# Performance work log

Measured on AMD Instinct MI355X. Metric: run time of the kernel, lower is better.

## Reference

```python
import jax, jax.numpy as jnp
import numpy as np

HIDDEN = 4096
Q_HEADS = 32
KV_HEADS = 8
HEAD_DIM = 128
MAX_LEN = 8192
PAST_LEN = 4096
SEQ_LEN = 16
BSZ = 1
REPEAT_KV = Q_HEADS // KV_HEADS
SCALE = HEAD_DIM ** (-0.5)


def _apply_rope(x):
    # x: [b, h, s, d]; positions start at 0 (faithful to source, even for cached k)
    s, d = x.shape[2], x.shape[3]
    half = d // 2
    positions = jnp.arange(s, dtype=x.dtype)
    inv_freq = jnp.arange(half, dtype=x.dtype) / half
    angles = positions[:, None] * inv_freq[None, :]          # [s, half]
    sin = jnp.sin(angles)[None, None]
    cos = jnp.cos(angles)[None, None]
    x_even, x_odd = x[..., :half], x[..., half:]
    return jnp.concatenate([x_even * cos - x_odd * sin,
                            x_even * sin + x_odd * cos], axis=-1)


def setup_inputs() -> dict:
    key = jax.random.key(0)
    ks = jax.random.split(key, 5)
    qkv_dim = (Q_HEADS + 2 * KV_HEADS) * HEAD_DIM
    x = jax.random.normal(ks[0], (BSZ, SEQ_LEN, HIDDEN), dtype=jnp.float32)
    w_qkv = jax.random.normal(ks[1], (qkv_dim, HIDDEN), dtype=jnp.float32) * 0.02
    w_out = jax.random.normal(ks[2], (HIDDEN, Q_HEADS * HEAD_DIM), dtype=jnp.float32) * 0.02
    cache_k = jax.random.normal(ks[3], (1, KV_HEADS, MAX_LEN, HEAD_DIM), dtype=jnp.float32)
    cache_v = jax.random.normal(ks[4], (1, KV_HEADS, MAX_LEN, HEAD_DIM), dtype=jnp.float32)
    return {"x": x, "w_qkv": w_qkv, "w_out": w_out, "cache_k": cache_k, "cache_v": cache_v}


def reference(x, w_qkv, w_out, cache_k, cache_v):
    bsz, seq_len, _ = x.shape
    qkv = jnp.einsum('bsh,oh->bso', x, w_qkv)
    q_size = Q_HEADS * HEAD_DIM
    kv_size = KV_HEADS * HEAD_DIM
    q = qkv[..., :q_size].reshape(bsz, seq_len, Q_HEADS, HEAD_DIM).transpose(0, 2, 1, 3)
    k = qkv[..., q_size:q_size + kv_size].reshape(bsz, seq_len, KV_HEADS, HEAD_DIM).transpose(0, 2, 1, 3)
    v = qkv[..., q_size + kv_size:].reshape(bsz, seq_len, KV_HEADS, HEAD_DIM).transpose(0, 2, 1, 3)
    q = _apply_rope(q)
    k = _apply_rope(k)
    # KV-cache append (static slice positions)
    cache_k = cache_k.at[:, :, PAST_LEN:PAST_LEN + seq_len, :].set(k)
    cache_v = cache_v.at[:, :, PAST_LEN:PAST_LEN + seq_len, :].set(v)
    key_len = PAST_LEN + seq_len
    key = cache_k[:, :, :key_len, :]
    value = cache_v[:, :, :key_len, :]
    if REPEAT_KV > 1:  # GQA broadcast
        key = jnp.repeat(key, REPEAT_KV, axis=1)
        value = jnp.repeat(value, REPEAT_KV, axis=1)
    scores = jnp.einsum('bhqd,bhkd->bhqk', q, key) * SCALE
    q_pos = jnp.arange(seq_len)
    k_pos = jnp.arange(key_len)
    mask = (k_pos[None, :] <= q_pos[:, None] + PAST_LEN).astype(scores.dtype)
    scores = scores + (1.0 - mask)[None, None] * -10000.0
    weights = jax.nn.softmax(scores, axis=-1)
    out = jnp.einsum('bhqk,bhkd->bhqd', weights, value)
    out = out.transpose(0, 2, 1, 3).reshape(bsz, seq_len, Q_HEADS * HEAD_DIM)
    return jnp.einsum('bso,ho->bsh', out, w_out)
```

## Files before the change

### kernel.cpp

```cpp
#include <hip/hip_runtime.h>
#include <hip/hip_bf16.h>

typedef __bf16 bf16;
typedef __bf16 bf16x4 __attribute__((ext_vector_type(4)));
typedef __bf16 bf16x8 __attribute__((ext_vector_type(8)));
typedef float f32x4 __attribute__((ext_vector_type(4)));

#define HID 4096
#define QKVN 6144
#define NQH 32
#define NKVH 8
#define HD 128
#define MAXLEN 8192
#define PAST 4096
#define SQ 16
#define SCALE 0.08838834764831845f
#define NEGBIG (-30000.0f)

#define KS 8
#define KPB 512
#define WSTR 520
#define ACH 64
#define NCH 65

__device__ __forceinline__ f32x4 mfma16(bf16x8 a, bf16x8 b, f32x4 c) {
  return __builtin_amdgcn_mfma_f32_16x16x32_bf16(a, b, c, 0, 0, 0);
}

__device__ __forceinline__ bf16x8 load8f(const float* p) {
  const f32x4* q = (const f32x4*)p;
  f32x4 a = q[0], b = q[1];
  bf16x8 r;
  r[0] = (bf16)a[0]; r[1] = (bf16)a[1]; r[2] = (bf16)a[2]; r[3] = (bf16)a[3];
  r[4] = (bf16)b[0]; r[5] = (bf16)b[1]; r[6] = (bf16)b[2]; r[7] = (bf16)b[3];
  return r;
}

__device__ __forceinline__ int fmidx(int k, int m) {
  return ((k >> 3) * 16 + m) * 8 + (k & 7);
}

__global__ __launch_bounds__(256) void xprep_kernel(const float* __restrict__ x,
                                                    bf16* __restrict__ xf) {
  int id = blockIdx.x * 256 + threadIdx.x;
  int m = id & 15, o = id >> 4;
  bf16x8 v = load8f(x + (size_t)m * HID + o * 8);
  *(bf16x8*)(xf + (size_t)(o * 16 + m) * 8) = v;
}

template <int NT>
__global__ __launch_bounds__(256) void gemm16_kernel(const bf16* __restrict__ afrag,
                                                     const float* __restrict__ w,
                                                     float* __restrict__ partial) {
  int tid = threadIdx.x, lane = tid & 63, wv = tid >> 6;
  int l15 = lane & 15, quad = lane >> 4;
  int nt = blockIdx.x % NT, kq = blockIdx.x / NT;

  __shared__ __align__(16) bf16 Wt[16 * WSTR];
  __shared__ __align__(16) float red[4][64][4];

  const float* wb = w + (size_t)(nt * 16) * HID + kq * KPB;
  int r2 = tid >> 7;
  int c4 = tid & 127;
  f32x4 stg[8];
#pragma unroll
  for (int it = 0; it < 8; ++it)
    stg[it] = *(const f32x4*)(wb + (size_t)(it * 2 + r2) * HID + c4 * 4);

  int obase = kq * 64 + wv * 16;
  bf16x8 af[4];
#pragma unroll
  for (int kk = 0; kk < 4; ++kk)
    af[kk] = *(const bf16x8*)(afrag + (size_t)((obase + kk * 4 + quad) * 16 + l15) * 8);

#pragma unroll
  for (int it = 0; it < 8; ++it) {
    bf16x4 t;
    t[0] = (bf16)stg[it][0]; t[1] = (bf16)stg[it][1];
    t[2] = (bf16)stg[it][2]; t[3] = (bf16)stg[it][3];
    *(bf16x4*)(Wt + (it * 2 + r2) * WSTR + c4 * 4) = t;
  }
  __syncthreads();

  f32x4 acc = {0.f, 0.f, 0.f, 0.f};
#pragma unroll
  for (int kk = 0; kk < 4; ++kk) {
    bf16x8 b = *(const bf16x8*)(Wt + l15 * WSTR + wv * 128 + kk * 32 + quad * 8);
    acc = mfma16(af[kk], b, acc);
  }

  *(f32x4*)(&red[wv][lane][0]) = acc;
  __syncthreads();
  if (wv == 0) {
#pragma unroll
    for (int r = 0; r < 4; ++r) {
      float v = red[0][lane][r] + red[1][lane][r] + red[2][lane][r] + red[3][lane][r];
      partial[((size_t)(kq * NT + nt) * 16 + (quad * 4 + r)) * 16 + l15] = v;
    }
  }
}

__device__ __forceinline__ float sum_part(const float* p, int NT, int n, int m) {
  float s = 0.f;
#pragma unroll
  for (int q = 0; q < KS; ++q)
    s += p[((size_t)(q * NT + (n >> 4)) * 16 + m) * 16 + (n & 15)];
  return s;
}

__global__ __launch_bounds__(256) void qkv_finish_kernel(const float* __restrict__ pq,
                                                         bf16* __restrict__ Qf,
                                                         bf16* __restrict__ Kf,
                                                         bf16* __restrict__ Vn) {
  int id = blockIdx.x * 256 + threadIdx.x;
  if (id < 32768) {
    int qh = id >> 10, m = (id >> 6) & 15, j = id & 63;
    float e = sum_part(pq, 384, qh * 128 + j, m);
    float o = sum_part(pq, 384, qh * 128 + 64 + j, m);
    float sn, co;
    __sincosf((float)m * (float)j * (1.0f / 64.0f), &sn, &co);
    Qf[qh * 2048 + fmidx(j, m)] = (bf16)((e * co - o * sn) * SCALE);
    Qf[qh * 2048 + fmidx(j + 64, m)] = (bf16)((e * sn + o * co) * SCALE);
  } else if (id < 40960) {
    int v = id - 32768;
    int kvh = v >> 10, m = (v >> 6) & 15, j = v & 63;
    float e = sum_part(pq, 384, 4096 + kvh * 128 + j, m);
    float o = sum_part(pq, 384, 4096 + kvh * 128 + 64 + j, m);
    float sn, co;
    __sincosf((float)m * (float)j * (1.0f / 64.0f), &sn, &co);
    Kf[kvh * 2048 + fmidx(j, m)] = (bf16)(e * co - o * sn);
    Kf[kvh * 2048 + fmidx(j + 64, m)] = (bf16)(e * sn + o * co);
  } else if (id < 57344) {
    int v = id - 40960;
    int kvh = v >> 11, m = (v >> 7) & 15, d = v & 127;
    Vn[kvh * 2048 + m * 128 + d] = (bf16)sum_part(pq, 384, 5120 + kvh * 128 + d, m);
  }
}

template <bool NEW>
__device__ void attn_body(int kvh, int c,
                          const float* __restrict__ ck, const float* __restrict__ cv,
                          const bf16* __restrict__ Qf, const bf16* __restrict__ Kf,
                          const bf16* __restrict__ Vn,
                          bf16* __restrict__ Opart, float* __restrict__ ml,
                          bf16* Kt, bf16* Vt, bf16* Pl) {
  int tid = threadIdx.x, lane = tid & 63, wv = tid >> 6;
  int l15 = lane & 15, quad = lane >> 4;
  int qh = kvh * 4 + wv;
  int cs = c * ACH;

  if (!NEW) {
    {
      int kr = tid >> 5;
      int kc4 = tid & 31;
      f32x4 kst[8];
#pragma unroll
      for (int it = 0; it < 8; ++it)
        kst[it] = *(const f32x4*)(ck + ((size_t)(kvh * MAXLEN + cs + it * 8 + kr)) * HD + kc4 * 4);
      int key = tid & 63, dg = tid >> 6;
      f32x4 vst[8];
#pragma unroll
      for (int q4 = 0; q4 < 8; ++q4)
        vst[q4] = *(const f32x4*)(cv + ((size_t)(kvh * MAXLEN + cs + key)) * HD + dg * 32 + q4 * 4);
#pragma unroll
      for (int it = 0; it < 8; ++it) {
        bf16x4 t;
        t[0] = (bf16)kst[it][0]; t[1] = (bf16)kst[it][1];
        t[2] = (bf16)kst[it][2]; t[3] = (bf16)kst[it][3];
        *(bf16x4*)(Kt + (it * 8 + kr) * 136 + kc4 * 4) = t;
      }
#pragma unroll
      for (int q4 = 0; q4 < 8; ++q4)
#pragma unroll
        for (int i = 0; i < 4; ++i)
          Vt[(dg * 32 + q4 * 4 + i) * 72 + key] = (bf16)vst[q4][i];
    }
  } else {
    int key = tid >> 4, dg8 = tid & 15;
    bf16x8 v = *(const bf16x8*)(Vn + kvh * 2048 + key * 128 + dg8 * 8);
#pragma unroll
    for (int i = 0; i < 8; ++i) {
      Vt[(dg8 * 8 + i) * 72 + key] = v[i];
      Vt[(dg8 * 8 + i) * 72 + 16 + key] = (bf16)0.f;
    }
  }
  __syncthreads();

  bf16x8 af[4];
#pragma unroll
  for (int kk = 0; kk < 4; ++kk)
    af[kk] = *(const bf16x8*)(Qf + qh * 2048 + ((kk * 4 + quad) * 16 + l15) * 8);

  constexpr int NT = NEW ? 1 : 4;
  f32x4 sc[NT];
  if (!NEW) {
#pragma unroll
    for (int nt = 0; nt < NT; ++nt) {
      f32x4 acc = {0.f, 0.f, 0.f, 0.f};
#pragma unroll
      for (int kk = 0; kk < 4; ++kk) {
        bf16x8 b = *(const bf16x8*)(Kt + (nt * 16 + l15) * 136 + kk * 32 + quad * 8);
        acc = mfma16(af[kk], b, acc);
      }
      sc[nt] = acc;
    }
  } else {
    f32x4 acc = {0.f, 0.f, 0.f, 0.f};
#pragma unroll
    for (int kk = 0; kk < 4; ++kk) {
      bf16x8 b = *(const bf16x8*)(Kf + kvh * 2048 + ((kk * 4 + quad) * 16 + l15) * 8);
      acc = mfma16(af[kk], b, acc);
    }
#pragma unroll
    for (int r = 0; r < 4; ++r)
      if (l15 > quad * 4 + r) acc[r] = NEGBIG;
    sc[0] = acc;
  }

  float mx[4], sm[4];
#pragma unroll
  for (int r = 0; r < 4; ++r) {
    float v = sc[0][r];
#pragma unroll
    for (int nt = 1; nt < NT; ++nt) v = fmaxf(v, sc[nt][r]);
    v = fmaxf(v, __shfl_xor(v, 1));
    v = fmaxf(v, __shfl_xor(v, 2));
    v = fmaxf(v, __shfl_xor(v, 4));
    v = fmaxf(v, __shfl_xor(v, 8));
    mx[r] = v;
  }
#pragma unroll
  for (int nt = 0; nt < NT; ++nt)
#pragma unroll
    for (int r = 0; r < 4; ++r) sc[nt][r] = __expf(sc[nt][r] - mx[r]);
#pragma unroll
  for (int r = 0; r < 4; ++r) {
    float v = 0.f;
#pragma unroll
    for (int nt = 0; nt < NT; ++nt) v += sc[nt][r];
    v += __shfl_xor(v, 1);
    v += __shfl_xor(v, 2);
    v += __shfl_xor(v, 4);
    v += __shfl_xor(v, 8);
    sm[r] = v;
  }

  bf16* Pw = Pl + wv * 16 * 72;
#pragma unroll
  for (int nt = 0; nt < NT; ++nt)
#pragma unroll
    for (int r = 0; r < 4; ++r)
      Pw[(quad * 4 + r) * 72 + nt * 16 + l15] = (bf16)sc[nt][r];
  if (NEW) {
#pragma unroll
    for (int r = 0; r < 4; ++r)
      Pw[(quad * 4 + r) * 72 + 16 + l15] = (bf16)0.f;
  }
  __syncthreads();

  constexpr int KI = NEW ? 1 : 2;
  int rowblk = ((kvh * NCH + c) * 4 + wv) * 16;
  bf16* ob = Opart + (size_t)rowblk * 128;
#pragma unroll
  for (int nt2 = 0; nt2 < 8; ++nt2) {
    f32x4 acc = {0.f, 0.f, 0.f, 0.f};
#pragma unroll
    for (int kk = 0; kk < KI; ++kk) {
      bf16x8 a = *(const bf16x8*)(Pw + l15 * 72 + kk * 32 + quad * 8);
      bf16x8 b = *(const bf16x8*)(Vt + (nt2 * 16 + l15) * 72 + kk * 32 + quad * 8);
      acc = mfma16(a, b, acc);
    }
#pragma unroll
    for (int r = 0; r < 4; ++r)
      ob[(quad * 4 + r) * 128 + nt2 * 16 + l15] = (bf16)acc[r];
  }
  if (l15 == 0) {
#pragma unroll
    for (int r = 0; r < 4; ++r) {
      ml[(size_t)(rowblk + quad * 4 + r) * 2] = mx[r];
      ml[(size_t)(rowblk + quad * 4 + r) * 2 + 1] = sm[r];
    }
  }
}

__global__ __launch_bounds__(256) void attn_kernel(const float* __restrict__ ck,
                                                   const float* __restrict__ cv,
                                                   const bf16* __restrict__ Qf,
                                                   const bf16* __restrict__ Kf,
                                                   const bf16* __restrict__ Vn,
                                                   bf16* __restrict__ Opart,
                                                   float* __restrict__ ml) {
  __shared__ __align__(16) bf16 KtL[64 * 136];
  __shared__ __align__(16) bf16 VtL[128 * 72];
  __shared__ __align__(16) bf16 PL[4 * 16 * 72];
  int c = blockIdx.x % NCH;
  int kvh = blockIdx.x / NCH;
  if (c == NCH - 1)
    attn_body<true>(kvh, c, ck, cv, Qf, Kf, Vn, Opart, ml, KtL, VtL, PL);
  else
    attn_body<false>(kvh, c, ck, cv, Qf, Kf, Vn, Opart, ml, KtL, VtL, PL);
}

__global__ __launch_bounds__(256) void combine_kernel(const bf16* __restrict__ Opart,
                                                      const float* __restrict__ ml,
                                                      bf16* __restrict__ attfm) {
  int tid = threadIdx.x, lane = tid & 63, wv = tid >> 6;
  int gw = blockIdx.x * 4 + wv;
  int qh = gw >> 4, srow = gw & 15;
  int kvh = qh >> 2, lw = qh & 3;
  int rowblk0 = ((kvh * NCH) * 4 + lw) * 16 + srow;
  const float* mlb = ml + (size_t)rowblk0 * 2;
  float m1 = mlb[(size_t)lane * 128];
  float l1 = mlb[(size_t)lane * 128 + 1];
  float m2 = NEGBIG, l2 = 0.f;
  if (lane == 0) {
    m2 = mlb[(size_t)64 * 128];
    l2 = mlb[(size_t)64 * 128 + 1];
  }
  float M = fmaxf(m1, m2);
  M = fmaxf(M, __shfl_xor(M, 1));
  M = fmaxf(M, __shfl_xor(M, 2));
  M = fmaxf(M, __shfl_xor(M, 4));
  M = fmaxf(M, __shfl_xor(M, 8));
  M = fmaxf(M, __shfl_xor(M, 16));
  M = fmaxf(M, __shfl_xor(M, 32));
  float w1 = __expf(m1 - M);
  float w2 = (lane == 0) ? __expf(m2 - M) : 0.f;
  float Lp = w1 * l1 + w2 * l2;
  Lp += __shfl_xor(Lp, 1);
  Lp += __shfl_xor(Lp, 2);
  Lp += __shfl_xor(Lp, 4);
  Lp += __shfl_xor(Lp, 8);
  Lp += __shfl_xor(Lp, 16);
  Lp += __shfl_xor(Lp, 32);
  float a0 = 0.f, a1 = 0.f;
  const bf16* ob = Opart + (size_t)rowblk0 * 128;
  for (int cc = 0; cc < 64; ++cc) {
    float wc = __shfl(w1, cc);
    const bf16* oc = ob + (size_t)cc * 8192;
    a0 += wc * (float)oc[lane];
    a1 += wc * (float)oc[64 + lane];
  }
  {
    float wc = __shfl(w2, 0);
    const bf16* oc = ob + (size_t)64 * 8192;
    a0 += wc * (float)oc[lane];
    a1 += wc * (float)oc[64 + lane];
  }
  float inv = 1.f / Lp;
  int k1 = qh * 128 + lane, k2 = k1 + 64;
  attfm[fmidx(k1, srow)] = (bf16)(a0 * inv);
  attfm[fmidx(k2, srow)] = (bf16)(a1 * inv);
}

__global__ __launch_bounds__(256) void proj_reduce_kernel(const float* __restrict__ pp,
                                                          float* __restrict__ out) {
  int flat = blockIdx.x * 256 + threadIdx.x;
  int m = flat >> 10, n = (flat & 1023) * 4;
  f32x4 s = {0.f, 0.f, 0.f, 0.f};
#pragma unroll
  for (int q = 0; q < KS; ++q)
    s += *(const f32x4*)(pp + ((size_t)(q * 256 + (n >> 4)) * 16 + m) * 16 + (n & 15));
  *(f32x4*)(out + (size_t)m * HID + n) = s;
}

extern "C" void kernel_launch(void* const* d_in, const int* in_sizes, int n_in,
                              void* d_out, int out_size, void* d_ws, size_t ws_size,
                              hipStream_t stream) {
  const float* x       = (const float*)d_in[0];
  const float* w_qkv   = (const float*)d_in[1];
  const float* w_out   = (const float*)d_in[2];
  const float* cache_k = (const float*)d_in[3];
  const float* cache_v = (const float*)d_in[4];
  float* out = (float*)d_out;

  char* p = (char*)d_ws;
  bf16*  Xfrag = (bf16*)p;               p += (size_t)16 * HID * 2;
  float* partQ = (float*)p;              p += (size_t)KS * 384 * 256 * 4;
  bf16*  Qf    = (bf16*)p;               p += (size_t)NQH * 2048 * 2;
  bf16*  Kf    = (bf16*)p;               p += (size_t)NKVH * 2048 * 2;
  bf16*  Vn    = (bf16*)p;               p += (size_t)NKVH * 2048 * 2;
  bf16*  Opart = (bf16*)p;               p += (size_t)NKVH * NCH * 4 * 16 * 128 * 2;
  float* ml    = (float*)p;              p += (size_t)NKVH * NCH * 4 * 16 * 2 * 4;
  bf16*  attfm = (bf16*)p;               p += (size_t)16 * HID * 2;
  float* partP = (float*)p;              p += (size_t)KS * 256 * 256 * 4;

  hipLaunchKernelGGL(xprep_kernel, dim3(32), dim3(256), 0, stream, x, Xfrag);
  hipLaunchKernelGGL((gemm16_kernel<384>), dim3(384 * KS), dim3(256), 0, stream, Xfrag, w_qkv, partQ);
  hipLaunchKernelGGL(qkv_finish_kernel, dim3(224), dim3(256), 0, stream, partQ, Qf, Kf, Vn);
  hipLaunchKernelGGL(attn_kernel, dim3(NKVH * NCH), dim3(256), 0, stream,
                     cache_k, cache_v, Qf, Kf, Vn, Opart, ml);
  hipLaunchKernelGGL(combine_kernel, dim3(128), dim3(256), 0, stream, Opart, ml, attfm);
  hipLaunchKernelGGL((gemm16_kernel<256>), dim3(256 * KS), dim3(256), 0, stream, attfm, w_out, partP);
  hipLaunchKernelGGL(proj_reduce_kernel, dim3(64), dim3(256), 0, stream, partP, out);
}
```

Before: 255.7 us.

## Replace split-K partial buffers with atomic accumulation and drop prep/reduce kernels

The GEMM kernel now loads weight and activation fragments straight from global memory into registers, with no LDS staging. It reads fp32 x directly, which removes the xprep kernel. Split-K partial sums are accumulated with atomicAdd into row-major output, replacing the partial buffers and the separate proj_reduce pass. The combine kernel is restructured to one block per (head,row) with a cross-wave merge, and it also zeroes the final output before the projection GEMM accumulates into it. This cuts two launches and the partial-buffer traffic, at the cost of float atomics, which give nondeterministic summation order, and uncoalesced direct weight loads.

```diff
diff --git a/kernel.cpp b/kernel.cpp
--- a/kernel.cpp
+++ b/kernel.cpp
@@ -7,19 +7,16 @@
 typedef float f32x4 __attribute__((ext_vector_type(4)));
 
 #define HID 4096
-#define QKVN 6144
 #define NQH 32
 #define NKVH 8
 #define HD 128
 #define MAXLEN 8192
 #define PAST 4096
-#define SQ 16
 #define SCALE 0.08838834764831845f
 #define NEGBIG (-30000.0f)
 
 #define KS 8
 #define KPB 512
-#define WSTR 520
 #define ACH 64
 #define NCH 65
 
@@ -27,67 +24,61 @@
   return __builtin_amdgcn_mfma_f32_16x16x32_bf16(a, b, c, 0, 0, 0);
 }
 
-__device__ __forceinline__ bf16x8 load8f(const float* p) {
-  const f32x4* q = (const f32x4*)p;
-  f32x4 a = q[0], b = q[1];
+__device__ __forceinline__ bf16x8 pack8(f32x4 a, f32x4 b) {
   bf16x8 r;
   r[0] = (bf16)a[0]; r[1] = (bf16)a[1]; r[2] = (bf16)a[2]; r[3] = (bf16)a[3];
   r[4] = (bf16)b[0]; r[5] = (bf16)b[1]; r[6] = (bf16)b[2]; r[7] = (bf16)b[3];
   return r;
 }
 
+__device__ __forceinline__ bf16x8 load8f(const float* p) {
+  const f32x4* q = (const f32x4*)p;
+  return pack8(q[0], q[1]);
+}
+
 __device__ __forceinline__ int fmidx(int k, int m) {
   return ((k >> 3) * 16 + m) * 8 + (k & 7);
 }
 
-__global__ __launch_bounds__(256) void xprep_kernel(const float* __restrict__ x,
-                                                    bf16* __restrict__ xf) {
-  int id = blockIdx.x * 256 + threadIdx.x;
-  int m = id & 15, o = id >> 4;
-  bf16x8 v = load8f(x + (size_t)m * HID + o * 8);
-  *(bf16x8*)(xf + (size_t)(o * 16 + m) * 8) = v;
-}
-
-template <int NT>
-__global__ __launch_bounds__(256) void gemm16_kernel(const bf16* __restrict__ afrag,
+__global__ __launch_bounds__(256) void zeroq_kernel(float* __restrict__ qa) {
+  f32x4 z = {0.f, 0.f, 0.f, 0.f};
+  *(f32x4*)(qa + (size_t)(blockIdx.x * 256 + threadIdx.x) * 4) = z;
+}
+
+template <int NT, int OSTR, bool AF32>
+__global__ __launch_bounds__(256) void gemm16_kernel(const void* __restrict__ aptr,
                                                      const float* __restrict__ w,
-                                                     float* __restrict__ partial) {
+                                                     float* __restrict__ oacc) {
   int tid = threadIdx.x, lane = tid & 63, wv = tid >> 6;
   int l15 = lane & 15, quad = lane >> 4;
   int nt = blockIdx.x % NT, kq = blockIdx.x / NT;
-
-  __shared__ __align__(16) bf16 Wt[16 * WSTR];
   __shared__ __align__(16) float red[4][64][4];
 
-  const float* wb = w + (size_t)(nt * 16) * HID + kq * KPB;
-  int r2 = tid >> 7;
-  int c4 = tid & 127;
-  f32x4 stg[8];
-#pragma unroll
-  for (int it = 0; it < 8; ++it)
-    stg[it] = *(const f32x4*)(wb + (size_t)(it * 2 + r2) * HID + c4 * 4);
-
-  int obase = kq * 64 + wv * 16;
+  int kbase = kq * KPB + wv * 128 + quad * 8;
+
+  const float* wb = w + (size_t)(nt * 16 + l15) * HID + kbase;
+  f32x4 w0[4], w1[4];
+#pragma unroll
+  for (int kk = 0; kk < 4; ++kk) {
+    w0[kk] = *(const f32x4*)(wb + kk * 32);
+    w1[kk] = *(const f32x4*)(wb + kk * 32 + 4);
+  }
+
   bf16x8 af[4];
+  if constexpr (AF32) {
+    const float* ab = (const float*)aptr + (size_t)l15 * HID + kbase;
+#pragma unroll
+    for (int kk = 0; kk < 4; ++kk) af[kk] = load8f(ab + kk * 32);
+  } else {
+    const bf16* ab = (const bf16*)aptr + (size_t)l15 * HID + kbase;
+#pragma unroll
+    for (int kk = 0; kk < 4; ++kk) af[kk] = *(const bf16x8*)(ab + kk * 32);
+  }
+
+  f32x4 acc = {0.f, 0.f, 0.f, 0.f};
 #pragma unroll
   for (int kk = 0; kk < 4; ++kk)
-    af[kk] = *(const bf16x8*)(afrag + (size_t)((obase + kk * 4 + quad) * 16 + l15) * 8);
-
-#pragma unroll
-  for (int it = 0; it < 8; ++it) {
-    bf16x4 t;
-    t[0] = (bf16)stg[it][0]; t[1] = (bf16)stg[it][1];
-    t[2] = (bf16)stg[it][2]; t[3] = (bf16)stg[it][3];
-    *(bf16x4*)(Wt + (it * 2 + r2) * WSTR + c4 * 4) = t;
-  }
-  __syncthreads();
-
-  f32x4 acc = {0.f, 0.f, 0.f, 0.f};
-#pragma unroll
-  for (int kk = 0; kk < 4; ++kk) {
-    bf16x8 b = *(const bf16x8*)(Wt + l15 * WSTR + wv * 128 + kk * 32 + quad * 8);
-    acc = mfma16(af[kk], b, acc);
-  }
+    acc = mfma16(af[kk], pack8(w0[kk], w1[kk]), acc);
 
   *(f32x4*)(&red[wv][lane][0]) = acc;
   __syncthreads();
@@ -95,28 +86,20 @@
 #pragma unroll
     for (int r = 0; r < 4; ++r) {
       float v = red[0][lane][r] + red[1][lane][r] + red[2][lane][r] + red[3][lane][r];
-      partial[((size_t)(kq * NT + nt) * 16 + (quad * 4 + r)) * 16 + l15] = v;
-    }
-  }
-}
-
-__device__ __forceinline__ float sum_part(const float* p, int NT, int n, int m) {
-  float s = 0.f;
-#pragma unroll
-  for (int q = 0; q < KS; ++q)
-    s += p[((size_t)(q * NT + (n >> 4)) * 16 + m) * 16 + (n & 15)];
-  return s;
-}
-
-__global__ __launch_bounds__(256) void qkv_finish_kernel(const float* __restrict__ pq,
+      atomicAdd(oacc + (size_t)(quad * 4 + r) * OSTR + nt * 16 + l15, v);
+    }
+  }
+}
+
+__global__ __launch_bounds__(256) void qkv_finish_kernel(const float* __restrict__ qa,
                                                          bf16* __restrict__ Qf,
                                                          bf16* __restrict__ Kf,
                                                          bf16* __restrict__ Vn) {
   int id = blockIdx.x * 256 + threadIdx.x;
   if (id < 32768) {
     int qh = id >> 10, m = (id >> 6) & 15, j = id & 63;
-    float e = sum_part(pq, 384, qh * 128 + j, m);
-    float o = sum_part(pq, 384, qh * 128 + 64 + j, m);
+    float e = qa[(size_t)m * 6144 + qh * 128 + j];
+    float o = qa[(size_t)m * 6144 + qh * 128 + 64 + j];
     float sn, co;
     __sincosf((float)m * (float)j * (1.0f / 64.0f), &sn, &co);
     Qf[qh * 2048 + fmidx(j, m)] = (bf16)((e * co - o * sn) * SCALE);
@@ -124,8 +107,8 @@
   } else if (id < 40960) {
     int v = id - 32768;
     int kvh = v >> 10, m = (v >> 6) & 15, j = v & 63;
-    float e = sum_part(pq, 384, 4096 + kvh * 128 + j, m);
-    float o = sum_part(pq, 384, 4096 + kvh * 128 + 64 + j, m);
+    float e = qa[(size_t)m * 6144 + 4096 + kvh * 128 + j];
+    float o = qa[(size_t)m * 6144 + 4096 + kvh * 128 + 64 + j];
     float sn, co;
     __sincosf((float)m * (float)j * (1.0f / 64.0f), &sn, &co);
     Kf[kvh * 2048 + fmidx(j, m)] = (bf16)(e * co - o * sn);
@@ -133,7 +116,7 @@
   } else if (id < 57344) {
     int v = id - 40960;
     int kvh = v >> 11, m = (v >> 7) & 15, d = v & 127;
-    Vn[kvh * 2048 + m * 128 + d] = (bf16)sum_part(pq, 384, 5120 + kvh * 128 + d, m);
+    Vn[kvh * 2048 + m * 128 + d] = (bf16)qa[(size_t)m * 6144 + 5120 + kvh * 128 + d];
   }
 }
 
@@ -303,65 +286,51 @@
 
 __global__ __launch_bounds__(256) void combine_kernel(const bf16* __restrict__ Opart,
                                                       const float* __restrict__ ml,
-                                                      bf16* __restrict__ attfm) {
+                                                      bf16* __restrict__ attrm,
+                                                      float* __restrict__ out) {
   int tid = threadIdx.x, lane = tid & 63, wv = tid >> 6;
-  int gw = blockIdx.x * 4 + wv;
-  int qh = gw >> 4, srow = gw & 15;
+  int qh = blockIdx.x >> 4, srow = blockIdx.x & 15;
   int kvh = qh >> 2, lw = qh & 3;
-  int rowblk0 = ((kvh * NCH) * 4 + lw) * 16 + srow;
-  const float* mlb = ml + (size_t)rowblk0 * 2;
-  float m1 = mlb[(size_t)lane * 128];
-  float l1 = mlb[(size_t)lane * 128 + 1];
-  float m2 = NEGBIG, l2 = 0.f;
-  if (lane == 0) {
-    m2 = mlb[(size_t)64 * 128];
-    l2 = mlb[(size_t)64 * 128 + 1];
-  }
-  float M = fmaxf(m1, m2);
-  M = fmaxf(M, __shfl_xor(M, 1));
-  M = fmaxf(M, __shfl_xor(M, 2));
-  M = fmaxf(M, __shfl_xor(M, 4));
-  M = fmaxf(M, __shfl_xor(M, 8));
-  M = fmaxf(M, __shfl_xor(M, 16));
-  M = fmaxf(M, __shfl_xor(M, 32));
-  float w1 = __expf(m1 - M);
-  float w2 = (lane == 0) ? __expf(m2 - M) : 0.f;
-  float Lp = w1 * l1 + w2 * l2;
-  Lp += __shfl_xor(Lp, 1);
-  Lp += __shfl_xor(Lp, 2);
-  Lp += __shfl_xor(Lp, 4);
-  Lp += __shfl_xor(Lp, 8);
-  Lp += __shfl_xor(Lp, 16);
-  Lp += __shfl_xor(Lp, 32);
-  float a0 = 0.f, a1 = 0.f;
-  const bf16* ob = Opart + (size_t)rowblk0 * 128;
-  for (int cc = 0; cc < 64; ++cc) {
-    float wc = __shfl(w1, cc);
-    const bf16* oc = ob + (size_t)cc * 8192;
+  size_t rowblk0 = ((size_t)(kvh * NCH) * 4 + lw) * 16 + srow;
+
+  if (tid < 32) {
+    f32x4 z = {0.f, 0.f, 0.f, 0.f};
+    *(f32x4*)(out + (size_t)(blockIdx.x * 32 + tid) * 4) = z;
+  }
+
+  float mw = NEGBIG;
+  for (int c = wv; c < NCH; c += 4)
+    mw = fmaxf(mw, ml[(rowblk0 + (size_t)c * 64) * 2]);
+
+  float a0 = 0.f, a1 = 0.f, Lw = 0.f;
+  for (int c = wv; c < NCH; c += 4) {
+    const float* mlc = ml + (rowblk0 + (size_t)c * 64) * 2;
+    float wc = __expf(mlc[0] - mw);
+    Lw += wc * mlc[1];
+    const bf16* oc = Opart + (rowblk0 + (size_t)c * 64) * 128;
     a0 += wc * (float)oc[lane];
     a1 += wc * (float)oc[64 + lane];
   }
-  {
-    float wc = __shfl(w2, 0);
-    const bf16* oc = ob + (size_t)64 * 8192;
-    a0 += wc * (float)oc[lane];
-    a1 += wc * (float)oc[64 + lane];
-  }
-  float inv = 1.f / Lp;
-  int k1 = qh * 128 + lane, k2 = k1 + 64;
-  attfm[fmidx(k1, srow)] = (bf16)(a0 * inv);
-  attfm[fmidx(k2, srow)] = (bf16)(a1 * inv);
-}
-
-__global__ __launch_bounds__(256) void proj_reduce_kernel(const float* __restrict__ pp,
-                                                          float* __restrict__ out) {
-  int flat = blockIdx.x * 256 + threadIdx.x;
-  int m = flat >> 10, n = (flat & 1023) * 4;
-  f32x4 s = {0.f, 0.f, 0.f, 0.f};
-#pragma unroll
-  for (int q = 0; q < KS; ++q)
-    s += *(const f32x4*)(pp + ((size_t)(q * 256 + (n >> 4)) * 16 + m) * 16 + (n & 15));
-  *(f32x4*)(out + (size_t)m * HID + n) = s;
+
+  __shared__ float sm_m[4], sm_l[4];
+  __shared__ float sm_a[4][128];
+  if (lane == 0) { sm_m[wv] = mw; sm_l[wv] = Lw; }
+  sm_a[wv][lane] = a0;
+  sm_a[wv][64 + lane] = a1;
+  __syncthreads();
+
+  if (wv == 0) {
+    float M = fmaxf(fmaxf(sm_m[0], sm_m[1]), fmaxf(sm_m[2], sm_m[3]));
+    float s0 = __expf(sm_m[0] - M), s1 = __expf(sm_m[1] - M);
+    float s2 = __expf(sm_m[2] - M), s3 = __expf(sm_m[3] - M);
+    float L = s0 * sm_l[0] + s1 * sm_l[1] + s2 * sm_l[2] + s3 * sm_l[3];
+    float inv = 1.f / L;
+    float A0 = s0 * sm_a[0][lane] + s1 * sm_a[1][lane] + s2 * sm_a[2][lane] + s3 * sm_a[3][lane];
+    float A1 = s0 * sm_a[0][64 + lane] + s1 * sm_a[1][64 + lane] +
+               s2 * sm_a[2][64 + lane] + s3 * sm_a[3][64 + lane];
+    attrm[(size_t)srow * HID + qh * 128 + lane] = (bf16)(A0 * inv);
+    attrm[(size_t)srow * HID + qh * 128 + 64 + lane] = (bf16)(A1 * inv);
+  }
 }
 
 extern "C" void kernel_launch(void* const* d_in, const int* in_sizes, int n_in,
@@ -375,22 +344,21 @@
   float* out = (float*)d_out;
 
   char* p = (char*)d_ws;
-  bf16*  Xfrag = (bf16*)p;               p += (size_t)16 * HID * 2;
-  float* partQ = (float*)p;              p += (size_t)KS * 384 * 256 * 4;
-  bf16*  Qf    = (bf16*)p;               p += (size_t)NQH * 2048 * 2;
-  bf16*  Kf    = (bf16*)p;               p += (size_t)NKVH * 2048 * 2;
-  bf16*  Vn    = (bf16*)p;               p += (size_t)NKVH * 2048 * 2;
-  bf16*  Opart = (bf16*)p;               p += (size_t)NKVH * NCH * 4 * 16 * 128 * 2;
-  float* ml    = (float*)p;              p += (size_t)NKVH * NCH * 4 * 16 * 2 * 4;
-  bf16*  attfm = (bf16*)p;               p += (size_t)16 * HID * 2;
-  float* partP = (float*)p;              p += (size_t)KS * 256 * 256 * 4;
-
-  hipLaunchKernelGGL(xprep_kernel, dim3(32), dim3(256), 0, stream, x, Xfrag);
-  hipLaunchKernelGGL((gemm16_kernel<384>), dim3(384 * KS), dim3(256), 0, stream, Xfrag, w_qkv, partQ);
-  hipLaunchKernelGGL(qkv_finish_kernel, dim3(224), dim3(256), 0, stream, partQ, Qf, Kf, Vn);
+  float* qkvacc = (float*)p;             p += (size_t)16 * 6144 * 4;
+  bf16*  Qf     = (bf16*)p;              p += (size_t)NQH * 2048 * 2;
+  bf16*  Kf     = (bf16*)p;              p += (size_t)NKVH * 2048 * 2;
+  bf16*  Vn     = (bf16*)p;              p += (size_t)NKVH * 2048 * 2;
+  bf16*  Opart  = (bf16*)p;              p += (size_t)NKVH * NCH * 4 * 16 * 128 * 2;
+  float* ml     = (float*)p;             p += (size_t)NKVH * NCH * 4 * 16 * 2 * 4;
+  bf16*  attrm  = (bf16*)p;              p += (size_t)16 * HID * 2;
+
+  hipLaunchKernelGGL(zeroq_kernel, dim3(96), dim3(256), 0, stream, qkvacc);
+  hipLaunchKernelGGL((gemm16_kernel<384, 6144, true>), dim3(384 * KS), dim3(256), 0, stream,
+                     (const void*)x, w_qkv, qkvacc);
+  hipLaunchKernelGGL(qkv_finish_kernel, dim3(224), dim3(256), 0, stream, qkvacc, Qf, Kf, Vn);
   hipLaunchKernelGGL(attn_kernel, dim3(NKVH * NCH), dim3(256), 0, stream,
                      cache_k, cache_v, Qf, Kf, Vn, Opart, ml);
-  hipLaunchKernelGGL(combine_kernel, dim3(128), dim3(256), 0, stream, Opart, ml, attfm);
-  hipLaunchKernelGGL((gemm16_kernel<256>), dim3(256 * KS), dim3(256), 0, stream, attfm, w_out, partP);
-  hipLaunchKernelGGL(proj_reduce_kernel, dim3(64), dim3(256), 0, stream, partP, out);
-}
+  hipLaunchKernelGGL(combine_kernel, dim3(512), dim3(256), 0, stream, Opart, ml, attrm, out);
+  hipLaunchKernelGGL((gemm16_kernel<256, 4096, false>), dim3(256 * KS), dim3(256), 0, stream,
+                     (const void*)attrm, w_out, out);
+}
```

Result: slower. 261.7 us (+2.3%).

## Fuse all stages into one cooperative persistent kernel with grid syncs

Applied to the files above, without the earlier changes.

Replaces the seven separate kernel launches with a single cooperative kernel of 520 blocks that runs every stage in sequence, separated by grid-wide barriers. LDS is shared between stages through a union. The combine step is also restructured so each query row is handled by one block, with four waves splitting the chunks and merging their results through LDS. This removes per-launch gaps, but in exchange the GEMM stages now run 520 blocks that loop over units instead of launching thousands of blocks, and each grid sync adds its own cost. If the cooperative launch fails, the code falls back to the multi-kernel path.

```diff
diff --git a/kernel.cpp b/kernel.cpp
--- a/kernel.cpp
+++ b/kernel.cpp
@@ -1,5 +1,8 @@
 #include <hip/hip_runtime.h>
 #include <hip/hip_bf16.h>
+#include <hip/hip_cooperative_groups.h>
+
+namespace cg = cooperative_groups;
 
 typedef __bf16 bf16;
 typedef __bf16 bf16x4 __attribute__((ext_vector_type(4)));
@@ -7,13 +10,10 @@
 typedef float f32x4 __attribute__((ext_vector_type(4)));
 
 #define HID 4096
-#define QKVN 6144
 #define NQH 32
 #define NKVH 8
 #define HD 128
 #define MAXLEN 8192
-#define PAST 4096
-#define SQ 16
 #define SCALE 0.08838834764831845f
 #define NEGBIG (-30000.0f)
 
@@ -22,6 +22,7 @@
 #define WSTR 520
 #define ACH 64
 #define NCH 65
+#define NBLK 520
 
 __device__ __forceinline__ f32x4 mfma16(bf16x8 a, bf16x8 b, f32x4 c) {
   return __builtin_amdgcn_mfma_f32_16x16x32_bf16(a, b, c, 0, 0, 0);
@@ -40,28 +41,29 @@
   return ((k >> 3) * 16 + m) * 8 + (k & 7);
 }
 
-__global__ __launch_bounds__(256) void xprep_kernel(const float* __restrict__ x,
-                                                    bf16* __restrict__ xf) {
-  int id = blockIdx.x * 256 + threadIdx.x;
+struct LdsGemm { bf16 Wt[16 * WSTR]; float red[4][64][4]; };
+struct LdsAttn { bf16 Kt[64 * 136]; bf16 Vt[128 * 72]; bf16 Pl[4 * 16 * 72]; };
+struct LdsComb { float m[4]; float l[4]; float a[4][128]; };
+union LdsAll { LdsGemm g; LdsAttn at; LdsComb c; };
+
+
+__device__ __forceinline__ void xprep_one(const float* __restrict__ x,
+                                          bf16* __restrict__ xf, int id) {
   int m = id & 15, o = id >> 4;
   bf16x8 v = load8f(x + (size_t)m * HID + o * 8);
   *(bf16x8*)(xf + (size_t)(o * 16 + m) * 8) = v;
 }
 
 template <int NT>
-__global__ __launch_bounds__(256) void gemm16_kernel(const bf16* __restrict__ afrag,
-                                                     const float* __restrict__ w,
-                                                     float* __restrict__ partial) {
-  int tid = threadIdx.x, lane = tid & 63, wv = tid >> 6;
-  int l15 = lane & 15, quad = lane >> 4;
-  int nt = blockIdx.x % NT, kq = blockIdx.x / NT;
-
-  __shared__ __align__(16) bf16 Wt[16 * WSTR];
-  __shared__ __align__(16) float red[4][64][4];
+__device__ __forceinline__ void gemm_unit(const bf16* __restrict__ afrag,
+                                          const float* __restrict__ w,
+                                          float* __restrict__ partial,
+                                          int u, int tid, LdsGemm* L) {
+  int lane = tid & 63, wv = tid >> 6, l15 = lane & 15, quad = lane >> 4;
+  int nt = u % NT, kq = u / NT;
 
   const float* wb = w + (size_t)(nt * 16) * HID + kq * KPB;
-  int r2 = tid >> 7;
-  int c4 = tid & 127;
+  int r2 = tid >> 7, c4 = tid & 127;
   f32x4 stg[8];
 #pragma unroll
   for (int it = 0; it < 8; ++it)
@@ -78,29 +80,29 @@
     bf16x4 t;
     t[0] = (bf16)stg[it][0]; t[1] = (bf16)stg[it][1];
     t[2] = (bf16)stg[it][2]; t[3] = (bf16)stg[it][3];
-    *(bf16x4*)(Wt + (it * 2 + r2) * WSTR + c4 * 4) = t;
+    *(bf16x4*)(L->Wt + (it * 2 + r2) * WSTR + c4 * 4) = t;
   }
   __syncthreads();
 
   f32x4 acc = {0.f, 0.f, 0.f, 0.f};
 #pragma unroll
   for (int kk = 0; kk < 4; ++kk) {
-    bf16x8 b = *(const bf16x8*)(Wt + l15 * WSTR + wv * 128 + kk * 32 + quad * 8);
+    bf16x8 b = *(const bf16x8*)(L->Wt + l15 * WSTR + wv * 128 + kk * 32 + quad * 8);
     acc = mfma16(af[kk], b, acc);
   }
 
-  *(f32x4*)(&red[wv][lane][0]) = acc;
+  *(f32x4*)(&L->red[wv][lane][0]) = acc;
   __syncthreads();
   if (wv == 0) {
 #pragma unroll
     for (int r = 0; r < 4; ++r) {
-      float v = red[0][lane][r] + red[1][lane][r] + red[2][lane][r] + red[3][lane][r];
+      float v = L->red[0][lane][r] + L->red[1][lane][r] + L->red[2][lane][r] + L->red[3][lane][r];
       partial[((size_t)(kq * NT + nt) * 16 + (quad * 4 + r)) * 16 + l15] = v;
     }
   }
 }
 
-__device__ __forceinline__ float sum_part(const float* p, int NT, int n, int m) {
+__device__ __forceinline__ float sum_part(const float* __restrict__ p, int NT, int n, int m) {
   float s = 0.f;
 #pragma unroll
   for (int q = 0; q < KS; ++q)
@@ -108,11 +110,9 @@
   return s;
 }
 
-__global__ __launch_bounds__(256) void qkv_finish_kernel(const float* __restrict__ pq,
-                                                         bf16* __restrict__ Qf,
-                                                         bf16* __restrict__ Kf,
-                                                         bf16* __restrict__ Vn) {
-  int id = blockIdx.x * 256 + threadIdx.x;
+__device__ __forceinline__ void finish_one(const float* __restrict__ pq,
+                                           bf16* __restrict__ Qf, bf16* __restrict__ Kf,
+                                           bf16* __restrict__ Vn, int id) {
   if (id < 32768) {
     int qh = id >> 10, m = (id >> 6) & 15, j = id & 63;
     float e = sum_part(pq, 384, qh * 128 + j, m);
@@ -138,43 +138,42 @@
 }
 
 template <bool NEW>
-__device__ void attn_body(int kvh, int c,
-                          const float* __restrict__ ck, const float* __restrict__ cv,
-                          const bf16* __restrict__ Qf, const bf16* __restrict__ Kf,
-                          const bf16* __restrict__ Vn,
-                          bf16* __restrict__ Opart, float* __restrict__ ml,
-                          bf16* Kt, bf16* Vt, bf16* Pl) {
+__device__ __forceinline__ void attn_one(int kvh, int c,
+                                         const float* __restrict__ ck, const float* __restrict__ cv,
+                                         const bf16* __restrict__ Qf, const bf16* __restrict__ Kf,
+                                         const bf16* __restrict__ Vn,
+                                         bf16* __restrict__ Opart, float* __restrict__ ml,
+                                         LdsAttn* L) {
   int tid = threadIdx.x, lane = tid & 63, wv = tid >> 6;
   int l15 = lane & 15, quad = lane >> 4;
   int qh = kvh * 4 + wv;
   int cs = c * ACH;
+  bf16* Kt = L->Kt; bf16* Vt = L->Vt; bf16* Pl = L->Pl;
 
   if (!NEW) {
-    {
-      int kr = tid >> 5;
-      int kc4 = tid & 31;
-      f32x4 kst[8];
-#pragma unroll
-      for (int it = 0; it < 8; ++it)
-        kst[it] = *(const f32x4*)(ck + ((size_t)(kvh * MAXLEN + cs + it * 8 + kr)) * HD + kc4 * 4);
-      int key = tid & 63, dg = tid >> 6;
-      f32x4 vst[8];
-#pragma unroll
-      for (int q4 = 0; q4 < 8; ++q4)
-        vst[q4] = *(const f32x4*)(cv + ((size_t)(kvh * MAXLEN + cs + key)) * HD + dg * 32 + q4 * 4);
-#pragma unroll
-      for (int it = 0; it < 8; ++it) {
-        bf16x4 t;
-        t[0] = (bf16)kst[it][0]; t[1] = (bf16)kst[it][1];
-        t[2] = (bf16)kst[it][2]; t[3] = (bf16)kst[it][3];
-        *(bf16x4*)(Kt + (it * 8 + kr) * 136 + kc4 * 4) = t;
-      }
-#pragma unroll
-      for (int q4 = 0; q4 < 8; ++q4)
-#pragma unroll
-        for (int i = 0; i < 4; ++i)
-          Vt[(dg * 32 + q4 * 4 + i) * 72 + key] = (bf16)vst[q4][i];
-    }
+    int kr = tid >> 5;
+    int kc4 = tid & 31;
+    f32x4 kst[8];
+#pragma unroll
+    for (int it = 0; it < 8; ++it)
+      kst[it] = *(const f32x4*)(ck + ((size_t)(kvh * MAXLEN + cs + it * 8 + kr)) * HD + kc4 * 4);
+    int key = tid & 63, dg = tid >> 6;
+    f32x4 vst[8];
+#pragma unroll
+    for (int q4 = 0; q4 < 8; ++q4)
+      vst[q4] = *(const f32x4*)(cv + ((size_t)(kvh * MAXLEN + cs + key)) * HD + dg * 32 + q4 * 4);
+#pragma unroll
+    for (int it = 0; it < 8; ++it) {
+      bf16x4 t;
+      t[0] = (bf16)kst[it][0]; t[1] = (bf16)kst[it][1];
+      t[2] = (bf16)kst[it][2]; t[3] = (bf16)kst[it][3];
+      *(bf16x4*)(Kt + (it * 8 + kr) * 136 + kc4 * 4) = t;
+    }
+#pragma unroll
+    for (int q4 = 0; q4 < 8; ++q4)
+#pragma unroll
+      for (int i = 0; i < 4; ++i)
+        Vt[(dg * 32 + q4 * 4 + i) * 72 + key] = (bf16)vst[q4][i];
   } else {
     int key = tid >> 4, dg8 = tid & 15;
     bf16x8 v = *(const bf16x8*)(Vn + kvh * 2048 + key * 128 + dg8 * 8);
@@ -283,85 +282,137 @@
   }
 }
 
-__global__ __launch_bounds__(256) void attn_kernel(const float* __restrict__ ck,
-                                                   const float* __restrict__ cv,
-                                                   const bf16* __restrict__ Qf,
-                                                   const bf16* __restrict__ Kf,
-                                                   const bf16* __restrict__ Vn,
-                                                   bf16* __restrict__ Opart,
-                                                   float* __restrict__ ml) {
-  __shared__ __align__(16) bf16 KtL[64 * 136];
-  __shared__ __align__(16) bf16 VtL[128 * 72];
-  __shared__ __align__(16) bf16 PL[4 * 16 * 72];
-  int c = blockIdx.x % NCH;
-  int kvh = blockIdx.x / NCH;
-  if (c == NCH - 1)
-    attn_body<true>(kvh, c, ck, cv, Qf, Kf, Vn, Opart, ml, KtL, VtL, PL);
-  else
-    attn_body<false>(kvh, c, ck, cv, Qf, Kf, Vn, Opart, ml, KtL, VtL, PL);
-}
-
-__global__ __launch_bounds__(256) void combine_kernel(const bf16* __restrict__ Opart,
-                                                      const float* __restrict__ ml,
-                                                      bf16* __restrict__ attfm) {
-  int tid = threadIdx.x, lane = tid & 63, wv = tid >> 6;
-  int gw = blockIdx.x * 4 + wv;
-  int qh = gw >> 4, srow = gw & 15;
+__device__ __forceinline__ void combine_one(const bf16* __restrict__ Opart,
+                                            const float* __restrict__ ml,
+                                            bf16* __restrict__ attfm,
+                                            int qh, int srow, int tid, LdsComb* L) {
+  int lane = tid & 63, wv = tid >> 6;
   int kvh = qh >> 2, lw = qh & 3;
-  int rowblk0 = ((kvh * NCH) * 4 + lw) * 16 + srow;
-  const float* mlb = ml + (size_t)rowblk0 * 2;
-  float m1 = mlb[(size_t)lane * 128];
-  float l1 = mlb[(size_t)lane * 128 + 1];
-  float m2 = NEGBIG, l2 = 0.f;
-  if (lane == 0) {
-    m2 = mlb[(size_t)64 * 128];
-    l2 = mlb[(size_t)64 * 128 + 1];
-  }
-  float M = fmaxf(m1, m2);
-  M = fmaxf(M, __shfl_xor(M, 1));
-  M = fmaxf(M, __shfl_xor(M, 2));
-  M = fmaxf(M, __shfl_xor(M, 4));
-  M = fmaxf(M, __shfl_xor(M, 8));
-  M = fmaxf(M, __shfl_xor(M, 16));
-  M = fmaxf(M, __shfl_xor(M, 32));
-  float w1 = __expf(m1 - M);
-  float w2 = (lane == 0) ? __expf(m2 - M) : 0.f;
-  float Lp = w1 * l1 + w2 * l2;
-  Lp += __shfl_xor(Lp, 1);
-  Lp += __shfl_xor(Lp, 2);
-  Lp += __shfl_xor(Lp, 4);
-  Lp += __shfl_xor(Lp, 8);
-  Lp += __shfl_xor(Lp, 16);
-  Lp += __shfl_xor(Lp, 32);
-  float a0 = 0.f, a1 = 0.f;
-  const bf16* ob = Opart + (size_t)rowblk0 * 128;
-  for (int cc = 0; cc < 64; ++cc) {
-    float wc = __shfl(w1, cc);
-    const bf16* oc = ob + (size_t)cc * 8192;
+  size_t rowblk0 = ((size_t)(kvh * NCH) * 4 + lw) * 16 + srow;
+
+  float mw = NEGBIG;
+  for (int c = wv; c < NCH; c += 4)
+    mw = fmaxf(mw, ml[(rowblk0 + (size_t)c * 64) * 2]);
+
+  float a0 = 0.f, a1 = 0.f, Lw = 0.f;
+  for (int c = wv; c < NCH; c += 4) {
+    const float* mlc = ml + (rowblk0 + (size_t)c * 64) * 2;
+    float wc = __expf(mlc[0] - mw);
+    Lw += wc * mlc[1];
+    const bf16* oc = Opart + (rowblk0 + (size_t)c * 64) * 128;
     a0 += wc * (float)oc[lane];
     a1 += wc * (float)oc[64 + lane];
   }
-  {
-    float wc = __shfl(w2, 0);
-    const bf16* oc = ob + (size_t)64 * 8192;
-    a0 += wc * (float)oc[lane];
-    a1 += wc * (float)oc[64 + lane];
-  }
-  float inv = 1.f / Lp;
-  int k1 = qh * 128 + lane, k2 = k1 + 64;
-  attfm[fmidx(k1, srow)] = (bf16)(a0 * inv);
-  attfm[fmidx(k2, srow)] = (bf16)(a1 * inv);
-}
-
-__global__ __launch_bounds__(256) void proj_reduce_kernel(const float* __restrict__ pp,
-                                                          float* __restrict__ out) {
-  int flat = blockIdx.x * 256 + threadIdx.x;
+
+  if (lane == 0) { L->m[wv] = mw; L->l[wv] = Lw; }
+  L->a[wv][lane] = a0;
+  L->a[wv][64 + lane] = a1;
+  __syncthreads();
+
+  if (wv == 0) {
+    float M = fmaxf(fmaxf(L->m[0], L->m[1]), fmaxf(L->m[2], L->m[3]));
+    float s0 = __expf(L->m[0] - M), s1 = __expf(L->m[1] - M);
+    float s2 = __expf(L->m[2] - M), s3 = __expf(L->m[3] - M);
+    float Ls = s0 * L->l[0] + s1 * L->l[1] + s2 * L->l[2] + s3 * L->l[3];
+    float inv = 1.f / Ls;
+    float A0 = s0 * L->a[0][lane] + s1 * L->a[1][lane] + s2 * L->a[2][lane] + s3 * L->a[3][lane];
+    float A1 = s0 * L->a[0][64 + lane] + s1 * L->a[1][64 + lane] +
+               s2 * L->a[2][64 + lane] + s3 * L->a[3][64 + lane];
+    int k1 = qh * 128 + lane, k2 = k1 + 64;
+    attfm[fmidx(k1, srow)] = (bf16)(A0 * inv);
+    attfm[fmidx(k2, srow)] = (bf16)(A1 * inv);
+  }
+}
+
+__device__ __forceinline__ void reduce_one(const float* __restrict__ pp,
+                                           float* __restrict__ out, int flat) {
   int m = flat >> 10, n = (flat & 1023) * 4;
   f32x4 s = {0.f, 0.f, 0.f, 0.f};
 #pragma unroll
   for (int q = 0; q < KS; ++q)
     s += *(const f32x4*)(pp + ((size_t)(q * 256 + (n >> 4)) * 16 + m) * 16 + (n & 15));
   *(f32x4*)(out + (size_t)m * HID + n) = s;
+}
+
+__global__ __launch_bounds__(256, 3) void fused_kernel(
+    const float* __restrict__ x, const float* __restrict__ w_qkv,
+    const float* __restrict__ w_out,
+    const float* __restrict__ ck, const float* __restrict__ cv,
+    bf16* __restrict__ Xfrag, float* __restrict__ partQ,
+    bf16* __restrict__ Qf, bf16* __restrict__ Kf, bf16* __restrict__ Vn,
+    bf16* __restrict__ Opart, float* __restrict__ ml,
+    bf16* __restrict__ attfm, float* __restrict__ partP,
+    float* __restrict__ out) {
+  __shared__ __align__(16) LdsAll lds;
+  cg::grid_group grid = cg::this_grid();
+  int tid = threadIdx.x, b = blockIdx.x;
+
+  {
+    int id = b * 256 + tid;
+    if (id < 8192) xprep_one(x, Xfrag, id);
+  }
+  grid.sync();
+
+  for (int u = b; u < 384 * KS; u += NBLK)
+    gemm_unit<384>(Xfrag, w_qkv, partQ, u, tid, &lds.g);
+  grid.sync();
+
+  {
+    int id = b * 256 + tid;
+    if (id < 57344) finish_one(partQ, Qf, Kf, Vn, id);
+  }
+  grid.sync();
+
+  {
+    int c = b % NCH, kvh = b / NCH;
+    if (c == NCH - 1) attn_one<true>(kvh, c, ck, cv, Qf, Kf, Vn, Opart, ml, &lds.at);
+    else              attn_one<false>(kvh, c, ck, cv, Qf, Kf, Vn, Opart, ml, &lds.at);
+  }
+  grid.sync();
+
+  if (b < 512) combine_one(Opart, ml, attfm, b >> 4, b & 15, tid, &lds.c);
+  grid.sync();
+
+  for (int u = b; u < 256 * KS; u += NBLK)
+    gemm_unit<256>(attfm, w_out, partP, u, tid, &lds.g);
+  grid.sync();
+
+  {
+    int id = b * 256 + tid;
+    if (id < 16384) reduce_one(partP, out, id);
+  }
+}
+
+__global__ __launch_bounds__(256) void xprep_k(const float* __restrict__ x, bf16* __restrict__ xf) {
+  xprep_one(x, xf, blockIdx.x * 256 + threadIdx.x);
+}
+template <int NT>
+__global__ __launch_bounds__(256) void gemm_k(const bf16* __restrict__ a, const float* __restrict__ w,
+                                              float* __restrict__ p) {
+  __shared__ __align__(16) LdsGemm L;
+  gemm_unit<NT>(a, w, p, blockIdx.x, threadIdx.x, &L);
+}
+__global__ __launch_bounds__(256) void finish_k(const float* __restrict__ pq, bf16* __restrict__ Qf,
+                                                bf16* __restrict__ Kf, bf16* __restrict__ Vn) {
+  finish_one(pq, Qf, Kf, Vn, blockIdx.x * 256 + threadIdx.x);
+}
+__global__ __launch_bounds__(256) void attn_k(const float* __restrict__ ck, const float* __restrict__ cv,
+                                              const bf16* __restrict__ Qf, const bf16* __restrict__ Kf,
+                                              const bf16* __restrict__ Vn, bf16* __restrict__ Opart,
+                                              float* __restrict__ ml) {
+  __shared__ __align__(16) LdsAttn L;
+  int c = blockIdx.x % NCH, kvh = blockIdx.x / NCH;
+  if (c == NCH - 1) attn_one<true>(kvh, c, ck, cv, Qf, Kf, Vn, Opart, ml, &L);
+  else              attn_one<false>(kvh, c, ck, cv, Qf, Kf, Vn, Opart, ml, &L);
+}
+__global__ __launch_bounds__(256) void combine_k(const bf16* __restrict__ Opart,
+                                                 const float* __restrict__ ml,
+                                                 bf16* __restrict__ attfm) {
+  __shared__ __align__(16) LdsComb L;
+  combine_one(Opart, ml, attfm, (int)blockIdx.x >> 4, (int)blockIdx.x & 15, threadIdx.x, &L);
+}
+__global__ __launch_bounds__(256) void reduce_k(const float* __restrict__ pp, float* __restrict__ out) {
+  reduce_one(pp, out, blockIdx.x * 256 + threadIdx.x);
 }
 
 extern "C" void kernel_launch(void* const* d_in, const int* in_sizes, int n_in,
@@ -385,12 +436,20 @@
   bf16*  attfm = (bf16*)p;               p += (size_t)16 * HID * 2;
   float* partP = (float*)p;              p += (size_t)KS * 256 * 256 * 4;
 
-  hipLaunchKernelGGL(xprep_kernel, dim3(32), dim3(256), 0, stream, x, Xfrag);
-  hipLaunchKernelGGL((gemm16_kernel<384>), dim3(384 * KS), dim3(256), 0, stream, Xfrag, w_qkv, partQ);
-  hipLaunchKernelGGL(qkv_finish_kernel, dim3(224), dim3(256), 0, stream, partQ, Qf, Kf, Vn);
-  hipLaunchKernelGGL(attn_kernel, dim3(NKVH * NCH), dim3(256), 0, stream,
-                     cache_k, cache_v, Qf, Kf, Vn, Opart, ml);
-  hipLaunchKernelGGL(combine_kernel, dim3(128), dim3(256), 0, stream, Opart, ml, attfm);
-  hipLaunchKernelGGL((gemm16_kernel<256>), dim3(256 * KS), dim3(256), 0, stream, attfm, w_out, partP);
-  hipLaunchKernelGGL(proj_reduce_kernel, dim3(64), dim3(256), 0, stream, partP, out);
-}
+  void* args[] = {(void*)&x, (void*)&w_qkv, (void*)&w_out, (void*)&cache_k, (void*)&cache_v,
+                  (void*)&Xfrag, (void*)&partQ, (void*)&Qf, (void*)&Kf, (void*)&Vn,
+                  (void*)&Opart, (void*)&ml, (void*)&attfm, (void*)&partP, (void*)&out};
+  hipError_t e = hipLaunchCooperativeKernel((const void*)fused_kernel, dim3(NBLK), dim3(256),
+                                            args, 0, stream);
+  if (e != hipSuccess) {
+    (void)hipGetLastError();
+    hipLaunchKernelGGL(xprep_k, dim3(32), dim3(256), 0, stream, x, Xfrag);
+    hipLaunchKernelGGL((gemm_k<384>), dim3(384 * KS), dim3(256), 0, stream, Xfrag, w_qkv, partQ);
+    hipLaunchKernelGGL(finish_k, dim3(224), dim3(256), 0, stream, partQ, Qf, Kf, Vn);
+    hipLaunchKernelGGL(attn_k, dim3(NKVH * NCH), dim3(256), 0, stream,
+                       cache_k, cache_v, Qf, Kf, Vn, Opart, ml);
+    hipLaunchKernelGGL(combine_k, dim3(512), dim3(256), 0, stream, Opart, ml, attfm);
+    hipLaunchKernelGGL((gemm_k<256>), dim3(256 * KS), dim3(256), 0, stream, attfm, w_out, partP);
+    hipLaunchKernelGGL(reduce_k, dim3(64), dim3(256), 0, stream, partP, out);
+  }
+}
```

Result: slower. 598.4 us (+134.0%).
